# Optimization experiments

Hardware: AMD Instinct MI355X
Metric: run time of the kernel (lower is better)

Reference implementation:

```python
import jax, jax.numpy as jnp
import numpy as np

HEAD_DIM = 64


def setup_inputs() -> dict:
    key = jax.random.key(0)
    ks = jax.random.split(key, 5)
    B, T, D = 2, 2048, 1024
    x = jax.random.normal(ks[0], (B, T, D), dtype=jnp.float32)
    # Linear weights stored as [in, out]; scaled like typical init.
    w_qkv = jax.random.normal(ks[1], (D, 3 * D), dtype=jnp.float32) / np.sqrt(D)
    b_qkv = jax.random.normal(ks[2], (3 * D,), dtype=jnp.float32) * 0.02
    w_o = jax.random.normal(ks[3], (D, D), dtype=jnp.float32) / np.sqrt(D)
    b_o = jax.random.normal(ks[4], (D,), dtype=jnp.float32) * 0.02
    return {"x": x, "w_qkv": w_qkv, "b_qkv": b_qkv, "w_o": w_o, "b_o": b_o,
            "window": 256}


def reference(x, w_qkv, b_qkv, w_o, b_o, window):
    B, T, D = x.shape
    H = D // HEAD_DIM
    qkv = x @ w_qkv + b_qkv                      # [B, T, 3D]
    q, k, v = jnp.split(qkv, 3, axis=-1)
    # [B, H, T, hd]
    q = q.reshape(B, T, H, HEAD_DIM).transpose(0, 2, 1, 3)
    k = k.reshape(B, T, H, HEAD_DIM).transpose(0, 2, 1, 3)
    v = v.reshape(B, T, H, HEAD_DIM).transpose(0, 2, 1, 3)
    # Causal band mask: key j valid for query i iff 0 <= i - j <= window.
    idx = jnp.arange(T)
    diff = idx[:, None] - idx[None, :]
    mask = (diff >= 0) & (diff <= window)        # [T, T] bool
    scale = 1.0 / np.sqrt(HEAD_DIM)
    scores = jnp.einsum("bhqd,bhkd->bhqk", q, k) * scale
    scores = jnp.where(mask, scores, -jnp.inf)
    attn = jax.nn.softmax(scores, axis=-1)       # each row has >=1 valid entry
    out = jnp.einsum("bhqk,bhkd->bhqd", attn, v)  # [B, H, T, hd]
    out = out.transpose(0, 2, 1, 3).reshape(B, T, D)
    return out @ w_o + b_o
```

## Files before the change

kernel.cpp:

```cpp
#include <hip/hip_runtime.h>

#define T_SEQ 2048
#define DMODEL 1024
#define NH 16
#define HD 64

typedef unsigned short u16;
typedef short s16;
typedef __attribute__((ext_vector_type(8))) unsigned short u16x8;
typedef __attribute__((ext_vector_type(4))) unsigned short u16x4;
typedef __attribute__((ext_vector_type(8))) short bf16x8;
typedef __attribute__((ext_vector_type(4))) float f32x4;

__device__ __forceinline__ u16 f2bf(float f) {
    union { float f; unsigned u; } v; v.f = f;
    unsigned r = v.u + 0x7fffu + ((v.u >> 16) & 1u);
    return (u16)(r >> 16);
}
__device__ __forceinline__ float bf2f(u16 u) {
    union { unsigned u; float f; } v; v.u = ((unsigned)u) << 16;
    return v.f;
}

__device__ __forceinline__ void gl_lds16(const u16* g, u16* l) {
    __builtin_amdgcn_global_load_lds(
        (const __attribute__((address_space(1))) unsigned int*)g,
        (__attribute__((address_space(3))) unsigned int*)l, 16, 0, 0);
}

__global__ __launch_bounds__(256) void convert_kernel(
    const float* __restrict__ in, u16* __restrict__ out, int n)
{
    int idx = (blockIdx.x * 256 + threadIdx.x) * 4;
    if (idx < n) {
        float4 v = *reinterpret_cast<const float4*>(&in[idx]);
        u16x4 o;
        o.x = f2bf(v.x); o.y = f2bf(v.y); o.z = f2bf(v.z); o.w = f2bf(v.w);
        *reinterpret_cast<u16x4*>(&out[idx]) = o;
    }
}

__global__ __launch_bounds__(256) void transpose_convert_kernel(
    const float* __restrict__ in, u16* __restrict__ out, int K, int N)
{
    __shared__ u16 tile[64][65];
    const int tid = threadIdx.x;
    const int k0 = blockIdx.y * 64, n0 = blockIdx.x * 64;
    const int r  = tid >> 2;
    const int c4 = (tid & 3) * 16;
    #pragma unroll
    for (int i = 0; i < 4; ++i) {
        float4 v = *reinterpret_cast<const float4*>(&in[(size_t)(k0 + r) * N + n0 + c4 + i * 4]);
        tile[c4 + i*4 + 0][r] = f2bf(v.x);
        tile[c4 + i*4 + 1][r] = f2bf(v.y);
        tile[c4 + i*4 + 2][r] = f2bf(v.z);
        tile[c4 + i*4 + 3][r] = f2bf(v.w);
    }
    __syncthreads();
    u16x8 o0, o1;
    #pragma unroll
    for (int i = 0; i < 8; ++i) o0[i] = tile[r][c4 + i];
    #pragma unroll
    for (int i = 0; i < 8; ++i) o1[i] = tile[r][c4 + 8 + i];
    *reinterpret_cast<u16x8*>(&out[(size_t)(n0 + r) * K + k0 + c4])     = o0;
    *reinterpret_cast<u16x8*>(&out[(size_t)(n0 + r) * K + k0 + c4 + 8]) = o1;
}

template<int BM, int BN, bool OUT_BF16>
__global__ __launch_bounds__(256) void gemm_mfma_kernel(
    const u16* __restrict__ A, const u16* __restrict__ BT,
    const float* __restrict__ bias,
    float* __restrict__ C, u16* __restrict__ Cb,
    int M, int N, int K)
{
    constexpr int BK = 32;
    __shared__ __align__(16) u16 As[BM * BK];
    __shared__ __align__(16) u16 Bs[BN * BK];

    const int tid  = threadIdx.x;
    const int wave = tid >> 6, lane = tid & 63;
    const int m0 = blockIdx.y * BM, n0 = blockIdx.x * BN;

    constexpr int WM = BM / 2, WN = BN / 2;
    constexpr int MF = WM / 16, NF = WN / 16;
    const int wm = (wave >> 1) * WM, wn = (wave & 1) * WN;
    const int l15 = lane & 15, l4 = lane >> 4;

    f32x4 acc[MF][NF];
    #pragma unroll
    for (int nf = 0; nf < NF; ++nf) {
        const float bv = bias[n0 + wn + nf * 16 + l15];
        #pragma unroll
        for (int mf = 0; mf < MF; ++mf)
            acc[mf][nf] = (f32x4){bv, bv, bv, bv};
    }

    const int srow = tid >> 2;
    const int soff = (tid & 3) * 8;

    for (int k0 = 0; k0 < K; k0 += BK) {
        __syncthreads();
        gl_lds16(&A[(size_t)(m0 + srow) * K + k0 + soff],       &As[(size_t)tid * 8]);
        gl_lds16(&A[(size_t)(m0 + 64 + srow) * K + k0 + soff],  &As[(size_t)(tid + 256) * 8]);
        gl_lds16(&BT[(size_t)(n0 + srow) * K + k0 + soff],      &Bs[(size_t)tid * 8]);
        if constexpr (BN == 128)
            gl_lds16(&BT[(size_t)(n0 + 64 + srow) * K + k0 + soff], &Bs[(size_t)(tid + 256) * 8]);
        __syncthreads();

        bf16x8 af[MF], bf[NF];
        #pragma unroll
        for (int mf = 0; mf < MF; ++mf)
            af[mf] = *reinterpret_cast<const bf16x8*>(&As[(wm + mf * 16 + l15) * BK + l4 * 8]);
        #pragma unroll
        for (int nf = 0; nf < NF; ++nf)
            bf[nf] = *reinterpret_cast<const bf16x8*>(&Bs[(wn + nf * 16 + l15) * BK + l4 * 8]);
        #pragma unroll
        for (int mf = 0; mf < MF; ++mf)
            #pragma unroll
            for (int nf = 0; nf < NF; ++nf)
                acc[mf][nf] = __builtin_amdgcn_mfma_f32_16x16x32_bf16(af[mf], bf[nf], acc[mf][nf], 0, 0, 0);
    }

    #pragma unroll
    for (int mf = 0; mf < MF; ++mf)
        #pragma unroll
        for (int nf = 0; nf < NF; ++nf) {
            const int col = n0 + wn + nf * 16 + l15;
            #pragma unroll
            for (int r = 0; r < 4; ++r) {
                const int row = m0 + wm + mf * 16 + l4 * 4 + r;
                if constexpr (OUT_BF16) Cb[(size_t)row * N + col] = f2bf(acc[mf][nf][r]);
                else                    C [(size_t)row * N + col] = acc[mf][nf][r];
            }
        }
}

__global__ __launch_bounds__(256) void swa_mfma_kernel(
    const u16* __restrict__ qkv, u16* __restrict__ out,
    const int* __restrict__ wptr)
{
    const int window = *wptr;
    const int qt = blockIdx.x;
    const int bh = blockIdx.y;
    const int b  = bh >> 4;
    const int h  = bh & (NH - 1);

    const int tid  = threadIdx.x;
    const int wave = tid >> 6, lane = tid & 63;
    const int l15  = lane & 15, l4 = lane >> 4;
    const int hoff = h * HD;

    __shared__ __align__(16) s16 Ks[64 * 64];
    __shared__ __align__(16) s16 Vt[64 * 64];
    __shared__ __align__(16) s16 Ps[64 * 64];

    auto swz = [](int row, int col) { return (row * 64 + col) ^ ((row & 7) << 3); };

    const size_t qgrow = (size_t)(b * T_SEQ + qt * 64 + wave * 16 + l15) * (3 * DMODEL) + hoff;
    const bf16x8 qf0 = *reinterpret_cast<const bf16x8*>(&qkv[qgrow + l4 * 8]);
    const bf16x8 qf1 = *reinterpret_cast<const bf16x8*>(&qkv[qgrow + 32 + l4 * 8]);

    f32x4 oacc[4];
    #pragma unroll
    for (int nf = 0; nf < 4; ++nf) oacc[nf] = (f32x4){0.f, 0.f, 0.f, 0.f};
    float m[4] = {-1e30f, -1e30f, -1e30f, -1e30f};
    float l[4] = {0.f, 0.f, 0.f, 0.f};

    const int lo = qt * 64 - window;
    const int cstart = (lo <= 0) ? 0 : (lo >> 6);

    const int kr = tid >> 3;
    const int kc = (tid & 7) * 8;

    for (int c = cstart; c <= qt; ++c) {
        const int j0 = c * 64;
        __syncthreads();
        #pragma unroll
        for (int pass = 0; pass < 2; ++pass) {
            const int row = kr + pass * 32;
            const size_t g = (size_t)(b * T_SEQ + j0 + row) * (3 * DMODEL) + hoff + kc;
            const bf16x8 kv8 = *reinterpret_cast<const bf16x8*>(&qkv[g + DMODEL]);
            const bf16x8 vv8 = *reinterpret_cast<const bf16x8*>(&qkv[g + 2 * DMODEL]);
            *reinterpret_cast<bf16x8*>(&Ks[swz(row, kc)]) = kv8;
            #pragma unroll
            for (int i = 0; i < 8; ++i)
                Vt[swz(kc + i, row)] = vv8[i];
        }
        __syncthreads();

        f32x4 sacc[4];
        #pragma unroll
        for (int nf = 0; nf < 4; ++nf) sacc[nf] = (f32x4){0.f, 0.f, 0.f, 0.f};
        #pragma unroll
        for (int nf = 0; nf < 4; ++nf) {
            const bf16x8 kf0 = *reinterpret_cast<const bf16x8*>(&Ks[swz(nf * 16 + l15, l4 * 8)]);
            const bf16x8 kf1 = *reinterpret_cast<const bf16x8*>(&Ks[swz(nf * 16 + l15, 32 + l4 * 8)]);
            sacc[nf] = __builtin_amdgcn_mfma_f32_16x16x32_bf16(qf0, kf0, sacc[nf], 0, 0, 0);
            sacc[nf] = __builtin_amdgcn_mfma_f32_16x16x32_bf16(qf1, kf1, sacc[nf], 0, 0, 0);
        }

        float p[4][4];
        #pragma unroll
        for (int r = 0; r < 4; ++r) {
            const int iq = qt * 64 + wave * 16 + l4 * 4 + r;
            float rmax = -1e30f;
            #pragma unroll
            for (int nf = 0; nf < 4; ++nf) {
                const int diff = iq - (j0 + nf * 16 + l15);
                const bool valid = (diff >= 0) && (diff <= window);
                const float s = valid ? sacc[nf][r] * 0.125f : -1e30f;
                p[r][nf] = s;
                rmax = fmaxf(rmax, s);
            }
            rmax = fmaxf(rmax, __shfl_xor(rmax, 1));
            rmax = fmaxf(rmax, __shfl_xor(rmax, 2));
            rmax = fmaxf(rmax, __shfl_xor(rmax, 4));
            rmax = fmaxf(rmax, __shfl_xor(rmax, 8));
            const float mn = fmaxf(m[r], rmax);
            const float rf = __expf(m[r] - mn);
            float rs = 0.f;
            #pragma unroll
            for (int nf = 0; nf < 4; ++nf) {
                const float e = __expf(p[r][nf] - mn);
                p[r][nf] = e;
                rs += e;
            }
            rs += __shfl_xor(rs, 1);
            rs += __shfl_xor(rs, 2);
            rs += __shfl_xor(rs, 4);
            rs += __shfl_xor(rs, 8);
            l[r] = l[r] * rf + rs;
            m[r] = mn;
            #pragma unroll
            for (int nf = 0; nf < 4; ++nf) oacc[nf][r] *= rf;
            #pragma unroll
            for (int nf = 0; nf < 4; ++nf)
                Ps[swz(wave * 16 + l4 * 4 + r, nf * 16 + l15)] = (s16)f2bf(p[r][nf]);
        }
        __syncthreads();

        #pragma unroll
        for (int ks = 0; ks < 2; ++ks) {
            const bf16x8 pa = *reinterpret_cast<const bf16x8*>(&Ps[swz(wave * 16 + l15, ks * 32 + l4 * 8)]);
            #pragma unroll
            for (int nf = 0; nf < 4; ++nf) {
                const bf16x8 vf = *reinterpret_cast<const bf16x8*>(&Vt[swz(nf * 16 + l15, ks * 32 + l4 * 8)]);
                oacc[nf] = __builtin_amdgcn_mfma_f32_16x16x32_bf16(pa, vf, oacc[nf], 0, 0, 0);
            }
        }
    }

    #pragma unroll
    for (int r = 0; r < 4; ++r) {
        const float inv = 1.f / l[r];
        const size_t orow = (size_t)(b * T_SEQ + qt * 64 + wave * 16 + l4 * 4 + r) * DMODEL + hoff;
        #pragma unroll
        for (int nf = 0; nf < 4; ++nf)
            out[orow + nf * 16 + l15] = f2bf(oacc[nf][r] * inv);
    }
}

extern "C" void kernel_launch(void* const* d_in, const int* in_sizes, int n_in,
                              void* d_out, int out_size, void* d_ws, size_t ws_size,
                              hipStream_t stream) {
    (void)in_sizes; (void)n_in; (void)out_size; (void)ws_size;

    const float* x     = (const float*)d_in[0];
    const float* w_qkv = (const float*)d_in[1];
    const float* b_qkv = (const float*)d_in[2];
    const float* w_o   = (const float*)d_in[3];
    const float* b_o   = (const float*)d_in[4];
    const int*   wnd   = (const int*)d_in[5];

    const int M = 2 * T_SEQ;

    char* w = (char*)d_ws;
    u16* qkvb  = (u16*)(w);
    u16* attb  = (u16*)(w + 24u * 1024 * 1024);
    u16* xb    = (u16*)(w + 32u * 1024 * 1024);
    u16* wqkvT = (u16*)(w + 40u * 1024 * 1024);
    u16* woT   = (u16*)(w + 46u * 1024 * 1024);

    dim3 blk(256);

    convert_kernel<<<dim3((M * DMODEL / 4 + 255) / 256), blk, 0, stream>>>(x, xb, M * DMODEL);
    transpose_convert_kernel<<<dim3(3 * DMODEL / 64, DMODEL / 64), blk, 0, stream>>>(
        w_qkv, wqkvT, DMODEL, 3 * DMODEL);
    transpose_convert_kernel<<<dim3(DMODEL / 64, DMODEL / 64), blk, 0, stream>>>(
        w_o, woT, DMODEL, DMODEL);

    gemm_mfma_kernel<128, 128, true><<<dim3(3 * DMODEL / 128, M / 128), blk, 0, stream>>>(
        xb, wqkvT, b_qkv, nullptr, qkvb, M, 3 * DMODEL, DMODEL);

    swa_mfma_kernel<<<dim3(T_SEQ / 64, 2 * NH), blk, 0, stream>>>(qkvb, attb, wnd);

    gemm_mfma_kernel<128, 64, false><<<dim3(DMODEL / 64, M / 128), blk, 0, stream>>>(
        attb, woT, b_o, (float*)d_out, nullptr, M, DMODEL, DMODEL);
}
```

Measured before the change: 176.6 us.

## Fuse x fp32-to-bf16 conversion into QKV GEMM, retile out-proj, reswizzle V

Drops the separate convert kernel and has the QKV GEMM load fp32 x directly, converting to bf16 in registers before storing to LDS. This removes one launch and a round trip through an intermediate bf16 buffer, but the A-tile loads are now synchronous register loads instead of direct global-to-LDS transfers. The output projection switches from 128x64 to 128x128 tiles, which halves its grid to 256 blocks. The transposed V tile in attention gets a new XOR swizzle meant to reduce LDS bank conflicts on the scattered transpose writes.

```diff
diff --git a/kernel.cpp b/kernel.cpp
--- a/kernel.cpp
+++ b/kernel.cpp
@@ -8,7 +8,6 @@
 typedef unsigned short u16;
 typedef short s16;
 typedef __attribute__((ext_vector_type(8))) unsigned short u16x8;
-typedef __attribute__((ext_vector_type(4))) unsigned short u16x4;
 typedef __attribute__((ext_vector_type(8))) short bf16x8;
 typedef __attribute__((ext_vector_type(4))) float f32x4;
 
@@ -17,27 +16,20 @@
     unsigned r = v.u + 0x7fffu + ((v.u >> 16) & 1u);
     return (u16)(r >> 16);
 }
-__device__ __forceinline__ float bf2f(u16 u) {
-    union { unsigned u; float f; } v; v.u = ((unsigned)u) << 16;
-    return v.f;
+
+__device__ __forceinline__ bf16x8 f2bf8(float4 a, float4 b) {
+    bf16x8 r;
+    r[0] = (s16)f2bf(a.x); r[1] = (s16)f2bf(a.y);
+    r[2] = (s16)f2bf(a.z); r[3] = (s16)f2bf(a.w);
+    r[4] = (s16)f2bf(b.x); r[5] = (s16)f2bf(b.y);
+    r[6] = (s16)f2bf(b.z); r[7] = (s16)f2bf(b.w);
+    return r;
 }
 
 __device__ __forceinline__ void gl_lds16(const u16* g, u16* l) {
     __builtin_amdgcn_global_load_lds(
         (const __attribute__((address_space(1))) unsigned int*)g,
         (__attribute__((address_space(3))) unsigned int*)l, 16, 0, 0);
-}
-
-__global__ __launch_bounds__(256) void convert_kernel(
-    const float* __restrict__ in, u16* __restrict__ out, int n)
-{
-    int idx = (blockIdx.x * 256 + threadIdx.x) * 4;
-    if (idx < n) {
-        float4 v = *reinterpret_cast<const float4*>(&in[idx]);
-        u16x4 o;
-        o.x = f2bf(v.x); o.y = f2bf(v.y); o.z = f2bf(v.z); o.w = f2bf(v.w);
-        *reinterpret_cast<u16x4*>(&out[idx]) = o;
-    }
 }
 
 __global__ __launch_bounds__(256) void transpose_convert_kernel(
@@ -66,9 +58,9 @@
     *reinterpret_cast<u16x8*>(&out[(size_t)(n0 + r) * K + k0 + c4 + 8]) = o1;
 }
 
-template<int BM, int BN, bool OUT_BF16>
+template<int BM, int BN, bool A_FP32, bool OUT_BF16>
 __global__ __launch_bounds__(256) void gemm_mfma_kernel(
-    const u16* __restrict__ A, const u16* __restrict__ BT,
+    const void* __restrict__ Aptr, const u16* __restrict__ BT,
     const float* __restrict__ bias,
     float* __restrict__ C, u16* __restrict__ Cb,
     int M, int N, int K)
@@ -98,13 +90,29 @@
     const int srow = tid >> 2;
     const int soff = (tid & 3) * 8;
 
+    const float* Af = (const float*)Aptr;
+    const u16*   Ab = (const u16*)Aptr;
+
     for (int k0 = 0; k0 < K; k0 += BK) {
-        __syncthreads();
-        gl_lds16(&A[(size_t)(m0 + srow) * K + k0 + soff],       &As[(size_t)tid * 8]);
-        gl_lds16(&A[(size_t)(m0 + 64 + srow) * K + k0 + soff],  &As[(size_t)(tid + 256) * 8]);
+        bf16x8 acv0, acv1;
+        if constexpr (A_FP32) {
+            const float* p0 = &Af[(size_t)(m0 + srow) * K + k0 + soff];
+            const float* p1 = &Af[(size_t)(m0 + 64 + srow) * K + k0 + soff];
+            acv0 = f2bf8(*reinterpret_cast<const float4*>(p0),
+                         *reinterpret_cast<const float4*>(p0 + 4));
+            acv1 = f2bf8(*reinterpret_cast<const float4*>(p1),
+                         *reinterpret_cast<const float4*>(p1 + 4));
+        }
+        __syncthreads();
+        if constexpr (A_FP32) {
+            *reinterpret_cast<bf16x8*>(&As[(size_t)tid * 8]) = acv0;
+            *reinterpret_cast<bf16x8*>(&As[(size_t)(tid + 256) * 8]) = acv1;
+        } else {
+            gl_lds16(&Ab[(size_t)(m0 + srow) * K + k0 + soff],      &As[(size_t)tid * 8]);
+            gl_lds16(&Ab[(size_t)(m0 + 64 + srow) * K + k0 + soff], &As[(size_t)(tid + 256) * 8]);
+        }
         gl_lds16(&BT[(size_t)(n0 + srow) * K + k0 + soff],      &Bs[(size_t)tid * 8]);
-        if constexpr (BN == 128)
-            gl_lds16(&BT[(size_t)(n0 + 64 + srow) * K + k0 + soff], &Bs[(size_t)(tid + 256) * 8]);
+        gl_lds16(&BT[(size_t)(n0 + 64 + srow) * K + k0 + soff], &Bs[(size_t)(tid + 256) * 8]);
         __syncthreads();
 
         bf16x8 af[MF], bf[NF];
@@ -155,6 +163,7 @@
     __shared__ __align__(16) s16 Ps[64 * 64];
 
     auto swz = [](int row, int col) { return (row * 64 + col) ^ ((row & 7) << 3); };
+    auto vtx = [](int d, int k) { return d * 64 + (((k >> 3) ^ (d >> 3)) & 7) * 8 + (k & 7); };
 
     const size_t qgrow = (size_t)(b * T_SEQ + qt * 64 + wave * 16 + l15) * (3 * DMODEL) + hoff;
     const bf16x8 qf0 = *reinterpret_cast<const bf16x8*>(&qkv[qgrow + l4 * 8]);
@@ -184,7 +193,7 @@
             *reinterpret_cast<bf16x8*>(&Ks[swz(row, kc)]) = kv8;
             #pragma unroll
             for (int i = 0; i < 8; ++i)
-                Vt[swz(kc + i, row)] = vv8[i];
+                Vt[vtx(kc + i, row)] = vv8[i];
         }
         __syncthreads();
 
@@ -244,7 +253,7 @@
             const bf16x8 pa = *reinterpret_cast<const bf16x8*>(&Ps[swz(wave * 16 + l15, ks * 32 + l4 * 8)]);
             #pragma unroll
             for (int nf = 0; nf < 4; ++nf) {
-                const bf16x8 vf = *reinterpret_cast<const bf16x8*>(&Vt[swz(nf * 16 + l15, ks * 32 + l4 * 8)]);
+                const bf16x8 vf = *reinterpret_cast<const bf16x8*>(&Vt[vtx(nf * 16 + l15, ks * 32 + l4 * 8)]);
                 oacc[nf] = __builtin_amdgcn_mfma_f32_16x16x32_bf16(pa, vf, oacc[nf], 0, 0, 0);
             }
         }
@@ -277,23 +286,21 @@
     char* w = (char*)d_ws;
     u16* qkvb  = (u16*)(w);
     u16* attb  = (u16*)(w + 24u * 1024 * 1024);
-    u16* xb    = (u16*)(w + 32u * 1024 * 1024);
-    u16* wqkvT = (u16*)(w + 40u * 1024 * 1024);
-    u16* woT   = (u16*)(w + 46u * 1024 * 1024);
+    u16* wqkvT = (u16*)(w + 32u * 1024 * 1024);
+    u16* woT   = (u16*)(w + 38u * 1024 * 1024);
 
     dim3 blk(256);
 
-    convert_kernel<<<dim3((M * DMODEL / 4 + 255) / 256), blk, 0, stream>>>(x, xb, M * DMODEL);
     transpose_convert_kernel<<<dim3(3 * DMODEL / 64, DMODEL / 64), blk, 0, stream>>>(
         w_qkv, wqkvT, DMODEL, 3 * DMODEL);
     transpose_convert_kernel<<<dim3(DMODEL / 64, DMODEL / 64), blk, 0, stream>>>(
         w_o, woT, DMODEL, DMODEL);
 
-    gemm_mfma_kernel<128, 128, true><<<dim3(3 * DMODEL / 128, M / 128), blk, 0, stream>>>(
-        xb, wqkvT, b_qkv, nullptr, qkvb, M, 3 * DMODEL, DMODEL);
+    gemm_mfma_kernel<128, 128, true, true><<<dim3(3 * DMODEL / 128, M / 128), blk, 0, stream>>>(
+        x, wqkvT, b_qkv, nullptr, qkvb, M, 3 * DMODEL, DMODEL);
 
     swa_mfma_kernel<<<dim3(T_SEQ / 64, 2 * NH), blk, 0, stream>>>(qkvb, attb, wnd);
 
-    gemm_mfma_kernel<128, 64, false><<<dim3(DMODEL / 64, M / 128), blk, 0, stream>>>(
+    gemm_mfma_kernel<128, 128, false, false><<<dim3(DMODEL / 128, M / 128), blk, 0, stream>>>(
         attb, woT, b_o, (float*)d_out, nullptr, M, DMODEL, DMODEL);
 }
```

After: 184.4 us. +4.4%, slower.
